# Performance work log

Hardware: AMD Instinct MI355X
Metric: run time of the kernel (lower is better)

The kernel has to match this reference:

```python
import jax, jax.numpy as jnp
import numpy as np

B, S, N_ITEMS, E, H, L, DFF = 32, 512, 2048, 512, 8, 2, 2048
DK = E // H
EPS = 1e-5


def setup_inputs() -> dict:
    key = jax.random.key(0)
    ks = jax.random.split(key, 32)
    sc = 0.02
    p = {
        'input_seq': jax.random.normal(ks[0], (B, S, N_ITEMS), jnp.float32),
        'emb_W': jax.random.normal(ks[1], (N_ITEMS, E), jnp.float32) * sc,
        'emb_b': jnp.zeros((E,), jnp.float32),
        'pos_emb': jax.random.normal(ks[2], (S, E), jnp.float32) * sc,
        'Wq': jax.random.normal(ks[3], (L, E, E), jnp.float32) * sc,
        'bq': jnp.zeros((L, E), jnp.float32),
        'Wk': jax.random.normal(ks[4], (L, E, E), jnp.float32) * sc,
        'bk': jnp.zeros((L, E), jnp.float32),
        'Wv': jax.random.normal(ks[5], (L, E, E), jnp.float32) * sc,
        'bv': jnp.zeros((L, E), jnp.float32),
        'Wo': jax.random.normal(ks[6], (L, E, E), jnp.float32) * sc,
        'bo': jnp.zeros((L, E), jnp.float32),
        'ln1_g': jnp.ones((L, E), jnp.float32),
        'ln1_b': jnp.zeros((L, E), jnp.float32),
        'W1': jax.random.normal(ks[7], (L, E, DFF), jnp.float32) * sc,
        'b1': jnp.zeros((L, DFF), jnp.float32),
        'W2': jax.random.normal(ks[8], (L, DFF, E), jnp.float32) * sc,
        'b2': jnp.zeros((L, E), jnp.float32),
        'ln2_g': jnp.ones((L, E), jnp.float32),
        'ln2_b': jnp.zeros((L, E), jnp.float32),
        'fc_W': jax.random.normal(ks[9], (E, 1), jnp.float32) * sc,
        'fc_b': jnp.zeros((1,), jnp.float32),
    }
    return p


def _layernorm(x, g, b):
    m = jnp.mean(x, axis=-1, keepdims=True)
    v = jnp.mean(jnp.square(x - m), axis=-1, keepdims=True)
    return (x - m) * jax.lax.rsqrt(v + EPS) * g + b


def reference(input_seq, emb_W, emb_b, pos_emb, Wq, bq, Wk, bk, Wv, bv, Wo, bo,
              ln1_g, ln1_b, W1, b1, W2, b2, ln2_g, ln2_b, fc_W, fc_b):
    x = input_seq @ emb_W + emb_b          # [B,S,E]
    x = x + pos_emb[None, :, :]
    tril = jnp.tril(jnp.ones((S, S), jnp.float32))  # causal lower-triangular
    for l in range(L):
        # --- self attention (faithful: tril BEFORE scale, zeros not -inf) ---
        q = (x @ Wq[l] + bq[l]).reshape(B, S, H, DK).transpose(0, 2, 1, 3)
        k = (x @ Wk[l] + bk[l]).reshape(B, S, H, DK).transpose(0, 2, 1, 3)
        v = (x @ Wv[l] + bv[l]).reshape(B, S, H, DK).transpose(0, 2, 1, 3)
        scores = jnp.einsum('bhqd,bhkd->bhqk', q, k)
        scores = (scores * tril) / np.sqrt(DK)
        probs = jax.nn.softmax(scores, axis=-1)
        attn = jnp.einsum('bhqk,bhkd->bhqd', probs, v)  # [B,H,S,DK]
        attn = attn.transpose(0, 2, 1, 3).reshape(B, S, E)
        attn = attn @ Wo[l] + bo[l]
        # faithful source bug: `self_attention(x,x,x)[0]` -> batch 0 only,
        # broadcast over all batches in the residual add
        attended0 = attn[0]                 # [S,E]
        x = _layernorm(x + attended0[None, :, :], ln1_g[l], ln1_b[l])
        # --- feed forward ---
        ff = jax.nn.relu(x @ W1[l] + b1[l]) @ W2[l] + b2[l]
        x = _layernorm(x + ff, ln2_g[l], ln2_b[l])
    out = (x @ fc_W + fc_b).squeeze(-1)     # [B,S]
    return out
```

## Files before the change

### kernel.cpp

```cpp
#include <hip/hip_runtime.h>


typedef __bf16 bf16;
typedef __bf16 bf16x8 __attribute__((ext_vector_type(8)));
typedef __bf16 bf16x4 __attribute__((ext_vector_type(4)));
typedef float  f32x4  __attribute__((ext_vector_type(4)));

#define SEQ 512

__device__ __forceinline__ void gl2lds16(const bf16* g, void* l) {
    __builtin_amdgcn_global_load_lds(
        (const __attribute__((address_space(1))) void*)g,
        (__attribute__((address_space(3))) void*)l, 16, 0, 0);
}

template<int N> __device__ __forceinline__ void waitvm() {
    if constexpr (N == 0)      asm volatile("s_waitcnt vmcnt(0)" ::: "memory");
    else if constexpr (N == 2) asm volatile("s_waitcnt vmcnt(2)" ::: "memory");
    else if constexpr (N == 3) asm volatile("s_waitcnt vmcnt(3)" ::: "memory");
    else if constexpr (N == 4) asm volatile("s_waitcnt vmcnt(4)" ::: "memory");
    else if constexpr (N == 5) asm volatile("s_waitcnt vmcnt(5)" ::: "memory");
    else if constexpr (N == 6) asm volatile("s_waitcnt vmcnt(6)" ::: "memory");
    else if constexpr (N == 8) asm volatile("s_waitcnt vmcnt(8)" ::: "memory");
    else static_assert(N == 0, "unsupported waitvm");
}

__global__ __launch_bounds__(512, 1)
void fattn(const bf16* __restrict__ qkv,
           const bf16* __restrict__ VT,
           bf16* __restrict__ attn0b)
{
    __shared__ __align__(1024) char smem[65536 + 65536 + 8192];
    char* Ks = smem;
    char* Vs = smem + 65536;
    const int h = blockIdx.y;
    const int q0 = blockIdx.x * 128;
    const int tid = threadIdx.x, lane = tid & 63, wv = tid >> 6;
    const int fr = lane & 15, fc = lane >> 4;
    char* Ps = smem + 131072 + wv * 1024;

    {
        const bf16* Kg = qkv + 512 + h * 64;
        #pragma unroll
        for (int p = 0; p < 8; ++p) {
            int row = p * 64 + (tid >> 3);
            int ch  = tid & 7;
            gl2lds16(Kg + (long long)row * 1536 + ((ch ^ (row & 7)) * 8),
                     Ks + p * 8192 + tid * 16);
        }
        const bf16* Vg = VT + (long long)h * 64 * 512;
        #pragma unroll
        for (int p = 0; p < 8; ++p) {
            int row = p * 8 + (tid >> 6);
            int ch  = tid & 63;
            int chg = (ch & ~7) | ((ch & 7) ^ (row & 7));
            gl2lds16(Vg + (long long)row * 512 + chg * 8,
                     Vs + p * 8192 + tid * 16);
        }
    }
    const int q0w = q0 + wv * 16;
    const int qg  = q0w + fr;
    bf16x8 qf[2];
    #pragma unroll
    for (int w = 0; w < 2; ++w)
        qf[w] = *(const bf16x8*)(qkv + (long long)qg * 1536 + h * 64 + w * 32 + fc * 8);

    asm volatile("s_waitcnt vmcnt(0)" ::: "memory");
    __builtin_amdgcn_s_barrier();
    asm volatile("" ::: "memory");

    f32x4 s[32] = {};
    #pragma unroll
    for (int kt = 0; kt < 32; ++kt) {
        #pragma unroll
        for (int w = 0; w < 2; ++w) {
            int row = kt * 16 + fr;
            bf16x8 kf = *(const bf16x8*)(Ks + row * 128 +
                                         (((w * 4 + fc) ^ (row & 7)) * 16));
            s[kt] = __builtin_amdgcn_mfma_f32_16x16x32_bf16(kf, qf[w], s[kt], 0, 0, 0);
        }
    }

    float mx = -3.4e38f;
    #pragma unroll
    for (int kt = 0; kt < 32; ++kt)
        #pragma unroll
        for (int rr = 0; rr < 4; ++rr) {
            int k = kt * 16 + fc * 4 + rr;
            float v = (k <= qg) ? s[kt][rr] * 0.125f : 0.0f;
            s[kt][rr] = v;
            mx = fmaxf(mx, v);
        }
    mx = fmaxf(mx, __shfl_xor(mx, 16));
    mx = fmaxf(mx, __shfl_xor(mx, 32));
    float sum = 0.f;
    #pragma unroll
    for (int kt = 0; kt < 32; ++kt)
        #pragma unroll
        for (int rr = 0; rr < 4; ++rr) {
            float e = __expf(s[kt][rr] - mx);
            s[kt][rr] = e;
            sum += e;
        }
    sum += __shfl_xor(sum, 16);
    sum += __shfl_xor(sum, 32);
    const float inv = 1.0f / sum;

    f32x4 o[4] = {};
    #pragma unroll
    for (int kt2 = 0; kt2 < 16; ++kt2) {
        bf16x4 u0, u1;
        #pragma unroll
        for (int rr = 0; rr < 4; ++rr) {
            u0[rr] = (bf16)(s[2 * kt2][rr] * inv);
            u1[rr] = (bf16)(s[2 * kt2 + 1][rr] * inv);
        }
        *(bf16x4*)(Ps + fr * 64 + ((fc ^ (fr & 7)) * 8))       = u0;
        *(bf16x4*)(Ps + fr * 64 + (((4 + fc) ^ (fr & 7)) * 8)) = u1;
        __threadfence_block();
        bf16x4 lo = *(const bf16x4*)(Ps + fr * 64 + (((2 * fc) ^ (fr & 7)) * 8));
        bf16x4 hi = *(const bf16x4*)(Ps + fr * 64 + (((2 * fc + 1) ^ (fr & 7)) * 8));
        bf16x8 pf;
        pf[0] = lo[0]; pf[1] = lo[1]; pf[2] = lo[2]; pf[3] = lo[3];
        pf[4] = hi[0]; pf[5] = hi[1]; pf[6] = hi[2]; pf[7] = hi[3];
        #pragma unroll
        for (int n = 0; n < 4; ++n) {
            int row = n * 16 + fr;
            int ch  = kt2 * 4 + fc;
            int chs = (ch & ~7) | ((ch & 7) ^ (row & 7));
            bf16x8 vf = *(const bf16x8*)(Vs + row * 1024 + chs * 16);
            o[n] = __builtin_amdgcn_mfma_f32_16x16x32_bf16(pf, vf, o[n], 0, 0, 0);
        }
    }

    #pragma unroll
    for (int n = 0; n < 4; ++n)
        #pragma unroll
        for (int rr = 0; rr < 4; ++rr) {
            int qrow = q0w + fc * 4 + rr;
            attn0b[(long long)qrow * 512 + h * 64 + n * 16 + fr] = (bf16)o[n][rr];
        }
}

template<int BN, int ACT, int POS>
__global__ __launch_bounds__(512, 1)
void mg8(const bf16* __restrict__ Ab, int lda,
         const bf16* __restrict__ Bt, int ldb,
         const float* __restrict__ bias, const float* __restrict__ pos,
         bf16* __restrict__ Cb, int ldc, int K)
{
    constexpr int BM = 256;
    constexpr int APASS = 2;
    constexpr int BPASS = BN / 128;
    constexpr int AHB = BM * 64;
    constexpr int BHB = BN * 64;
    constexpr int WM = (BN == 256 ? 2 : 4), WN = 8 / WM;
    constexpr int MR = BM / WM / 16;
    constexpr int NR = BN / WN / 16;
    __shared__ __align__(1024) char smem[4 * AHB + 4 * BHB];
    char* ABase = smem;
    char* BBase = smem + 4 * AHB;

    const int gx = gridDim.x, gy = gridDim.y;
    const int nwg = gx * gy;
    const int b = blockIdx.y * gx + blockIdx.x;
    const int q = nwg >> 3, r = nwg & 7;
    const int xcd = b & 7, loc = b >> 3;
    const int wg = (xcd < r ? xcd * (q + 1) : r * (q + 1) + (xcd - r) * q) + loc;
    const int bx = wg % gx, by = wg / gx;
    const int row0 = by * BM, col0 = bx * BN;

    const int tid = threadIdx.x, lane = tid & 63, wv = tid >> 6;
    const int wr = (WM == 2 ? (wv >> 2) : (wv >> 1));
    const int wc = (WM == 2 ? (wv & 3) : (wv & 1));
    const int fr = lane & 15, fc = lane >> 4;

    const bf16* aS[APASS];
    #pragma unroll
    for (int p = 0; p < APASS; ++p) {
        int cL = p * 512 + tid;
        int row = cL >> 2, ch = cL & 3;
        aS[p] = Ab + (long long)(row0 + row) * lda + ((ch ^ (row & 3)) * 8);
    }
    const bf16* bS[BPASS];
    #pragma unroll
    for (int p = 0; p < BPASS; ++p) {
        int cL = p * 512 + tid;
        int row = cL >> 2, ch = cL & 3;
        bS[p] = Bt + (long long)(col0 + row) * ldb + ((ch ^ (row & 3)) * 8);
    }
    int aOff[MR], bOff[NR];
    #pragma unroll
    for (int m = 0; m < MR; ++m) {
        int row = wr * (BM / WM) + m * 16 + fr;
        aOff[m] = row * 64 + ((fc ^ (row & 3)) * 16);
    }
    #pragma unroll
    for (int n = 0; n < NR; ++n) {
        int row = wc * (BN / WN) + n * 16 + fr;
        bOff[n] = row * 64 + ((fc ^ (row & 3)) * 16);
    }

    auto stagePart = [&](int j) {
        const int tau = j >> 2, kh = (j >> 1) & 1, d = tau & 1;
        const int koff = tau * 64 + kh * 32;
        if (!(j & 1)) {
            char* dst = ABase + (d * 2 + kh) * AHB + wv * 1024;
            #pragma unroll
            for (int p = 0; p < APASS; ++p)
                gl2lds16(aS[p] + koff, dst + p * 8192);
        } else {
            char* dst = BBase + (d * 2 + kh) * BHB + wv * 1024;
            #pragma unroll
            for (int p = 0; p < BPASS; ++p)
                gl2lds16(bS[p] + koff, dst + p * 8192);
        }
    };

    const int nt = K >> 6;
    const int T = 4 * nt;
    #pragma unroll
    for (int j = 0; j < 6; ++j)
        if (j < T) stagePart(j);
    waitvm<2 * (APASS + BPASS)>();
    __builtin_amdgcn_s_barrier();

    f32x4 acc[MR][NR] = {};
    const int NPH = 2 * nt;
    for (int g = 0; g < NPH; ++g) {
        const int tau = g >> 1, ks = g & 1, d = tau & 1;

        const char* as = ABase + (d * 2 + ks) * AHB;
        const char* bs = BBase + (d * 2 + ks) * BHB;
        bf16x8 a[MR], b2[NR];
        #pragma unroll
        for (int m = 0; m < MR; ++m) a[m] = *(const bf16x8*)(as + aOff[m]);
        #pragma unroll
        for (int n = 0; n < NR; ++n) b2[n] = *(const bf16x8*)(bs + bOff[n]);

        if (2 * g + 6 < T) stagePart(2 * g + 6);
        if (2 * g + 7 < T) stagePart(2 * g + 7);

        __builtin_amdgcn_s_setprio(1);
        #pragma unroll
        for (int m = 0; m < MR; ++m)
            #pragma unroll
            for (int n = 0; n < NR; ++n)
                acc[m][n] = __builtin_amdgcn_mfma_f32_16x16x32_bf16(
                    a[m], b2[n], acc[m][n], 0, 0, 0);
        __builtin_amdgcn_s_setprio(0);

        const int rem = T - (2 * g + 4);
        if (rem >= 4)      waitvm<2 * (APASS + BPASS)>();
        else if (rem == 3) waitvm<2 * APASS + BPASS>();
        else if (rem == 2) waitvm<APASS + BPASS>();
        else if (rem == 1) waitvm<APASS>();
        else               waitvm<0>();
        __builtin_amdgcn_s_barrier();
    }

    float* st = (float*)(smem + wv * 4096);
    const int rowb = row0 + wr * (BM / WM);
    const int colb = col0 + wc * (BN / WN);
    #pragma unroll
    for (int m = 0; m < MR; ++m) {
        #pragma unroll
        for (int n = 0; n < NR; ++n) {
            int col = colb + n * 16 + fr;
            float bb = bias ? bias[col] : 0.f;
            #pragma unroll
            for (int rr = 0; rr < 4; ++rr) {
                float x = acc[m][n][rr] + bb;
                if constexpr (POS) {
                    int rowg = rowb + m * 16 + fc * 4 + rr;
                    x += pos[(rowg & 511) * 512 + col];
                }
                if constexpr (ACT) x = fmaxf(x, 0.f);
                st[(fc * 4 + rr) * 64 + n * 16 + fr] = x;
            }
        }
        #pragma unroll
        for (int sgi = 0; sgi < 2; ++sgi) {
            int row = sgi * 8 + (lane >> 3);
            int c8 = (lane & 7) * 8;
            f32x4 u = *(const f32x4*)&st[row * 64 + c8];
            f32x4 v = *(const f32x4*)&st[row * 64 + c8 + 4];
            bf16x8 w8;
            w8[0] = (bf16)u[0]; w8[1] = (bf16)u[1];
            w8[2] = (bf16)u[2]; w8[3] = (bf16)u[3];
            w8[4] = (bf16)v[0]; w8[5] = (bf16)v[1];
            w8[6] = (bf16)v[2]; w8[7] = (bf16)v[3];
            *(bf16x8*)&Cb[(long long)(rowb + m * 16 + row) * ldc + colb + c8] = w8;
        }
    }
}

template<int BM, int BN, int ACT, int CMODE, int CAUSAL>
__global__ __launch_bounds__(256, 4)
void mgemm(const bf16* __restrict__ Ab, int lda, long long sA,
           const bf16* __restrict__ Bt, int ldb, long long sB,
           const float* __restrict__ bias,
           float* __restrict__ Cf, bf16* __restrict__ Cb, int ldc, long long sC,
           int K)
{
    static_assert(BM == 128 && (BN == 128 || BN == 64), "tile");
    const int gx = gridDim.x, gy = gridDim.y;
    const int nwg = gx * gy;
    const int b = blockIdx.y * gx + blockIdx.x;
    const int q = nwg >> 3, r = nwg & 7;
    const int xcd = b & 7, loc = b >> 3;
    const int wg = (xcd < r ? xcd * (q + 1) : r * (q + 1) + (xcd - r) * q) + loc;
    const int bx = wg % gx, by = wg / gx;
    if (CAUSAL && bx * BN > by * BM + (BM - 1)) return;

    constexpr int TM = BM / 32, TN = BN / 32;
    constexpr int AIT = BM / 64, BIT = BN / 64;
    constexpr int ABY = BM * 64;
    constexpr int BBY = BN * 64;
    __shared__ bf16 As[2 * BM * 32];
    __shared__ bf16 Bs[2 * BN * 32];
    char* AsB = (char*)As;
    char* BsB = (char*)Bs;
    const int tid = threadIdx.x;
    const int lane = tid & 63, wv = tid >> 6;
    const int wr = wv >> 1, wc = wv & 1;
    const int fr = lane & 15, fc = lane >> 4;
    const int row0 = by * BM, col0 = bx * BN;
    const int z = blockIdx.z;

    Ab += (long long)z * sA;
    Bt += (long long)z * sB;
    if constexpr (CMODE == 0) Cf += (long long)z * sC;
    else                      Cb += (long long)z * sC;

    f32x4 acc[TM][TN] = {};

    const bf16* aSrc[AIT];
    #pragma unroll
    for (int it = 0; it < AIT; ++it) {
        int cL = it * 256 + tid;
        int row = cL >> 2, ch = cL & 3;
        aSrc[it] = Ab + (long long)(row0 + row) * lda + ((ch ^ (row & 3)) * 8);
    }
    const bf16* bSrc[BIT];
    #pragma unroll
    for (int it = 0; it < BIT; ++it) {
        int cL = it * 256 + tid;
        int row = cL >> 2, ch = cL & 3;
        bSrc[it] = Bt + (long long)(col0 + row) * ldb + ((ch ^ (row & 3)) * 8);
    }
    int aOff[TM], bOff[TN];
    #pragma unroll
    for (int m = 0; m < TM; ++m) {
        int row = wr * (BM / 2) + m * 16 + fr;
        aOff[m] = row * 64 + ((fc ^ (row & 3)) * 16);
    }
    #pragma unroll
    for (int n = 0; n < TN; ++n) {
        int row = wc * (BN / 2) + n * 16 + fr;
        bOff[n] = row * 64 + ((fc ^ (row & 3)) * 16);
    }

    auto stageTo = [&](int buf, int kt) {
        #pragma unroll
        for (int it = 0; it < AIT; ++it)
            gl2lds16(aSrc[it] + kt, AsB + buf * ABY + it * 4096 + wv * 1024);
        #pragma unroll
        for (int it = 0; it < BIT; ++it)
            gl2lds16(bSrc[it] + kt, BsB + buf * BBY + it * 4096 + wv * 1024);
    };

    const int nt = K >> 5;
    stageTo(0, 0);
    asm volatile("s_waitcnt vmcnt(0)" ::: "memory");
    __builtin_amdgcn_s_barrier();
    asm volatile("" ::: "memory");

    int cur = 0;
    for (int t = 0; t < nt; ++t) {
        if (t + 1 < nt) stageTo(cur ^ 1, (t + 1) * 32);
        bf16x8 a[TM], b2[TN];
        #pragma unroll
        for (int m = 0; m < TM; ++m) a[m] = *(const bf16x8*)(AsB + cur * ABY + aOff[m]);
        #pragma unroll
        for (int n = 0; n < TN; ++n) b2[n] = *(const bf16x8*)(BsB + cur * BBY + bOff[n]);
        __builtin_amdgcn_s_setprio(1);
        #pragma unroll
        for (int m = 0; m < TM; ++m)
            #pragma unroll
            for (int n = 0; n < TN; ++n)
                acc[m][n] = __builtin_amdgcn_mfma_f32_16x16x32_bf16(a[m], b2[n], acc[m][n], 0, 0, 0);
        __builtin_amdgcn_s_setprio(0);
        if (t + 1 < nt) {
            asm volatile("s_waitcnt vmcnt(0)" ::: "memory");
            __builtin_amdgcn_s_barrier();
            asm volatile("" ::: "memory");
            cur ^= 1;
        }
    }

    #pragma unroll
    for (int n = 0; n < TN; ++n) {
        int col = col0 + wc * (BN / 2) + n * 16 + fr;
        float bb = bias ? bias[col] : 0.f;
        #pragma unroll
        for (int m = 0; m < TM; ++m) {
            int rbase = row0 + wr * (BM / 2) + m * 16 + fc * 4;
            #pragma unroll
            for (int rr = 0; rr < 4; ++rr) {
                float x = acc[m][n][rr] + bb;
                if constexpr (ACT) x = fmaxf(x, 0.f);
                long long ci = (long long)(rbase + rr) * ldc + col;
                if constexpr (CMODE == 0) Cf[ci] = x;
                else                      Cb[ci] = (bf16)x;
            }
        }
    }
}

__global__ __launch_bounds__(256)
void cvt_k(const float* __restrict__ in, bf16* __restrict__ outb, long long n8)
{
    long long i = (long long)blockIdx.x * 256 + threadIdx.x;
    const long long stride = (long long)gridDim.x * 256;
    for (; i < n8; i += stride) {
        const float* p = in + i * 8;
        float4 u = *(const float4*)p;
        float4 v = *(const float4*)(p + 4);
        bf16x8 w8;
        w8[0] = (bf16)u.x; w8[1] = (bf16)u.y; w8[2] = (bf16)u.z; w8[3] = (bf16)u.w;
        w8[4] = (bf16)v.x; w8[5] = (bf16)v.y; w8[6] = (bf16)v.z; w8[7] = (bf16)v.w;
        *(bf16x8*)(outb + i * 8) = w8;
    }
}

__global__ __launch_bounds__(256)
void wt_k(const float* __restrict__ W, bf16* __restrict__ WT, int K, int N)
{
    __shared__ float t[32][33];
    int n0 = blockIdx.x * 32, k0 = blockIdx.y * 32;
    int r = threadIdx.x >> 3, c4 = (threadIdx.x & 7) * 4;
    float4 v = *(const float4*)&W[(long long)(k0 + r) * N + n0 + c4];
    t[r][c4 + 0] = v.x; t[r][c4 + 1] = v.y;
    t[r][c4 + 2] = v.z; t[r][c4 + 3] = v.w;
    __syncthreads();
    int n = threadIdx.x >> 3, kk4 = (threadIdx.x & 7) * 4;
    bf16x4 o;
    o[0] = (bf16)t[kk4 + 0][n]; o[1] = (bf16)t[kk4 + 1][n];
    o[2] = (bf16)t[kk4 + 2][n]; o[3] = (bf16)t[kk4 + 3][n];
    *(bf16x4*)&WT[(long long)(n0 + n) * K + k0 + kk4] = o;
}

__global__ __launch_bounds__(512)
void packb_k(const float* __restrict__ bq, const float* __restrict__ bk,
             const float* __restrict__ bv, float* __restrict__ dst)
{
    int l = blockIdx.x, t = threadIdx.x;
    dst[l * 1536 + t]        = bq[l * 512 + t];
    dst[l * 1536 + 512 + t]  = bk[l * 512 + t];
    dst[l * 1536 + 1024 + t] = bv[l * 512 + t];
}

__global__ __launch_bounds__(256)
void vt_k(const bf16* __restrict__ qkv, bf16* __restrict__ VT)
{
    __shared__ bf16 t[64][80];
    int h = blockIdx.y, s0 = blockIdx.x * 64;
    int r = threadIdx.x >> 2, c16 = (threadIdx.x & 3) * 16;
    const bf16* src = qkv + (long long)(s0 + r) * 1536 + 1024 + h * 64 + c16;
    *(bf16x8*)&t[r][c16]     = *(const bf16x8*)src;
    *(bf16x8*)&t[r][c16 + 8] = *(const bf16x8*)(src + 8);
    __syncthreads();
    int d = r, seg = c16;
    bf16 tmp[16];
    #pragma unroll
    for (int j = 0; j < 16; ++j) tmp[j] = t[seg + j][d];
    bf16* dst = VT + ((long long)(h * 64 + d)) * 512 + s0 + seg;
    *(bf16x8*)dst       = *(bf16x8*)&tmp[0];
    *(bf16x8*)(dst + 8) = *(bf16x8*)&tmp[8];
}

__global__ __launch_bounds__(128)
void addln_k(bf16* __restrict__ xb, const bf16* __restrict__ res,
             unsigned resMask, const float* __restrict__ g,
             const float* __restrict__ bta)
{
    long long row = blockIdx.x;
    int tid = threadIdx.x;
    int c = tid * 4;
    bf16x4 xv4 = *(const bf16x4*)&xb[row * 512 + c];
    bf16x4 rv4 = *(const bf16x4*)&res[(long long)(blockIdx.x & resMask) * 512 + c];
    float x0 = (float)xv4[0] + (float)rv4[0];
    float x1 = (float)xv4[1] + (float)rv4[1];
    float x2 = (float)xv4[2] + (float)rv4[2];
    float x3 = (float)xv4[3] + (float)rv4[3];
    float s = x0 + x1 + x2 + x3;
    float qq = x0 * x0 + x1 * x1 + x2 * x2 + x3 * x3;
    #pragma unroll
    for (int off = 32; off; off >>= 1) {
        s += __shfl_xor(s, off);
        qq += __shfl_xor(qq, off);
    }
    __shared__ float rs[2], rq[2];
    if ((tid & 63) == 0) { rs[tid >> 6] = s; rq[tid >> 6] = qq; }
    __syncthreads();
    s = rs[0] + rs[1]; qq = rq[0] + rq[1];
    float mean = s * (1.0f / 512.0f);
    float var  = qq * (1.0f / 512.0f) - mean * mean;
    float rstd = rsqrtf(var + 1e-5f);
    float4 gv = *(const float4*)&g[c];
    float4 bv = *(const float4*)&bta[c];
    bf16x4 o4;
    o4[0] = (bf16)((x0 - mean) * rstd * gv.x + bv.x);
    o4[1] = (bf16)((x1 - mean) * rstd * gv.y + bv.y);
    o4[2] = (bf16)((x2 - mean) * rstd * gv.z + bv.z);
    o4[3] = (bf16)((x3 - mean) * rstd * gv.w + bv.w);
    *(bf16x4*)&xb[row * 512 + c] = o4;
}

__global__ __launch_bounds__(256)
void fc_k(const bf16* __restrict__ x, const float* __restrict__ w,
          const float* __restrict__ bb, float* __restrict__ out)
{
    int row  = blockIdx.x * 4 + (threadIdx.x >> 6);
    int lane = threadIdx.x & 63;
    const bf16* xr = x + (long long)row * 512;
    bf16x8 a8 = *(const bf16x8*)&xr[lane * 8];
    float4 w0 = *(const float4*)&w[lane * 8];
    float4 w1 = *(const float4*)&w[lane * 8 + 4];
    float s = (float)a8[0] * w0.x + (float)a8[1] * w0.y
            + (float)a8[2] * w0.z + (float)a8[3] * w0.w
            + (float)a8[4] * w1.x + (float)a8[5] * w1.y
            + (float)a8[6] * w1.z + (float)a8[7] * w1.w;
    #pragma unroll
    for (int off = 32; off; off >>= 1) s += __shfl_xor(s, off);
    if (lane == 0) out[row] = s + bb[0];
}

extern "C" void kernel_launch(void* const* d_in, const int* in_sizes, int n_in,
                              void* d_out, int out_size, void* d_ws, size_t ws_size,
                              hipStream_t stream)
{
    const float* input_seq = (const float*)d_in[0];
    const float* emb_W  = (const float*)d_in[1];
    const float* emb_b  = (const float*)d_in[2];
    const float* pos_emb= (const float*)d_in[3];
    const float* Wq = (const float*)d_in[4];
    const float* bq = (const float*)d_in[5];
    const float* Wk = (const float*)d_in[6];
    const float* bk = (const float*)d_in[7];
    const float* Wv = (const float*)d_in[8];
    const float* bv = (const float*)d_in[9];
    const float* Wo = (const float*)d_in[10];
    const float* bo = (const float*)d_in[11];
    const float* ln1_g = (const float*)d_in[12];
    const float* ln1_b = (const float*)d_in[13];
    const float* W1 = (const float*)d_in[14];
    const float* b1 = (const float*)d_in[15];
    const float* W2 = (const float*)d_in[16];
    const float* b2 = (const float*)d_in[17];
    const float* ln2_g = (const float*)d_in[18];
    const float* ln2_b = (const float*)d_in[19];
    const float* fcW = (const float*)d_in[20];
    const float* fcb = (const float*)d_in[21];
    float* out = (float*)d_out;

    char* w = (char*)d_ws;
    size_t off = 0;
    auto alloc = [&](size_t bytes) -> void* {
        off = (off + 255) & ~(size_t)255;
        void* p = w + off;
        off += bytes;
        return p;
    };
    bf16*  xb     = (bf16*) alloc(16384ull * 512 * 2);
    bf16*  embWT  = (bf16*) alloc(512ull * 2048 * 2);
    bf16*  qkvWT  = (bf16*) alloc(2ull * 1536 * 512 * 2);
    bf16*  WoT    = (bf16*) alloc(2ull * 512 * 512 * 2);
    bf16*  W1T    = (bf16*) alloc(2ull * 2048 * 512 * 2);
    bf16*  W2T    = (bf16*) alloc(2ull * 512 * 2048 * 2);
    float* qkvB   = (float*)alloc(2ull * 1536 * 4);
    off = (off + 255) & ~(size_t)255;
    char* dynp = w + off;
    bf16*  seqb     = (bf16*)dynp;
    bf16*  qkv      = (bf16*)dynp;
    bf16*  VT       = (bf16*)(dynp + 1572864);
    bf16*  attn0b   = (bf16*)(dynp + 1572864 + 524288);
    bf16*  attnout0b= (bf16*)(dynp + 1572864 + 524288 + 524288);
    bf16*  hidden = (bf16*)dynp;
    bf16*  ffout  = (bf16*)(dynp + 16384ull * 2048 * 2);

    dim3 blk(256);
    dim3 blk512(512);

    wt_k<<<dim3(16, 64), blk, 0, stream>>>(emb_W, embWT, 2048, 512);
    for (int l = 0; l < 2; ++l) {
        wt_k<<<dim3(16, 16), blk, 0, stream>>>(Wq + l * 262144, qkvWT + l * 786432,          512, 512);
        wt_k<<<dim3(16, 16), blk, 0, stream>>>(Wk + l * 262144, qkvWT + l * 786432 + 262144, 512, 512);
        wt_k<<<dim3(16, 16), blk, 0, stream>>>(Wv + l * 262144, qkvWT + l * 786432 + 524288, 512, 512);
        wt_k<<<dim3(16, 16), blk, 0, stream>>>(Wo + l * 262144, WoT + l * 262144, 512, 512);
        wt_k<<<dim3(64, 16), blk, 0, stream>>>(W1 + l * 1048576, W1T + l * 1048576, 512, 2048);
        wt_k<<<dim3(16, 64), blk, 0, stream>>>(W2 + l * 1048576, W2T + l * 1048576, 2048, 512);
    }
    packb_k<<<dim3(2), dim3(512), 0, stream>>>(bq, bk, bv, qkvB);
    cvt_k<<<dim3(2048), blk, 0, stream>>>(input_seq, seqb, 16384ll * 2048 / 8);

    mg8<128, 0, 1><<<dim3(4, 64), blk512, 0, stream>>>(
        seqb, 2048, embWT, 2048, emb_b, pos_emb, xb, 512, 2048);

    for (int l = 0; l < 2; ++l) {
        const bf16* qkvWT_l = qkvWT + l * 786432;
        const bf16* WoT_l   = WoT + l * 262144;
        const bf16* W1T_l   = W1T + l * 1048576;
        const bf16* W2T_l   = W2T + l * 1048576;

        mgemm<128, 128, 0, 1, 0><<<dim3(12, 4), blk, 0, stream>>>(
            xb, 512, 0, qkvWT_l, 512, 0, qkvB + l * 1536,
            nullptr, qkv, 1536, 0, 512);
        vt_k<<<dim3(8, 8), blk, 0, stream>>>(qkv, VT);
        fattn<<<dim3(4, 8), blk512, 0, stream>>>(qkv, VT, attn0b);
        mgemm<128, 128, 0, 1, 0><<<dim3(4, 4), blk, 0, stream>>>(
            attn0b, 512, 0, WoT_l, 512, 0, bo + l * 512, nullptr,
            attnout0b, 512, 0, 512);
        addln_k<<<dim3(16384), dim3(128), 0, stream>>>(
            xb, attnout0b, 511u, ln1_g + l * 512, ln1_b + l * 512);

        mg8<256, 1, 0><<<dim3(8, 64), blk512, 0, stream>>>(
            xb, 512, W1T_l, 512, b1 + l * 2048, nullptr, hidden, 2048, 512);
        mg8<128, 0, 0><<<dim3(4, 64), blk512, 0, stream>>>(
            hidden, 2048, W2T_l, 2048, b2 + l * 512, nullptr, ffout, 512, 2048);
        addln_k<<<dim3(16384), dim3(128), 0, stream>>>(
            xb, ffout, 0xffffffffu, ln2_g + l * 512, ln2_b + l * 512);
    }

    fc_k<<<dim3(4096), blk, 0, stream>>>(xb, fcW, fcb, out);
}
```

Before: 402.2 us.

## Fuse weight-prep launches into one kernel and shrink attention GEMM tiles

Merges the thirteen weight-transpose launches, the bias pack and the input fp32-to-bf16 conversion into a single table-driven kernel, so per-launch overhead and the tail gaps between many small kernels go away. It also halves the N tile of the QKV and output-projection GEMMs on the batch-0 path, which doubles their block counts so more CUs are busy on these small problems. The cost is a per-block lookup over the table and smaller tiles with less data reuse per block.

```diff
diff --git a/kernel.cpp b/kernel.cpp
--- a/kernel.cpp
+++ b/kernel.cpp
@@ -23,6 +23,67 @@
     else if constexpr (N == 6) asm volatile("s_waitcnt vmcnt(6)" ::: "memory");
     else if constexpr (N == 8) asm volatile("s_waitcnt vmcnt(8)" ::: "memory");
     else static_assert(N == 0, "unsupported waitvm");
+}
+
+struct WTab {
+    const float* src[13];
+    bf16*        dst[13];
+    int          K[13];
+    int          N[13];
+    int          base[13];
+    const float *bq, *bk, *bv;
+    float*       qkvB;
+    const float* cvtsrc;
+    bf16*        cvtdst;
+};
+
+__global__ __launch_bounds__(256)
+void wtall_k(WTab tab, int nTiles)
+{
+    const int b = blockIdx.x;
+    if (b < nTiles) {
+        int mi = 0;
+        #pragma unroll
+        for (int i = 1; i < 13; ++i)
+            if (b >= tab.base[i]) mi = i;
+        const int lt = b - tab.base[mi];
+        const int K = tab.K[mi], N = tab.N[mi];
+        const int tx = N >> 5;
+        const int n0 = (lt % tx) * 32, k0 = (lt / tx) * 32;
+        const float* W = tab.src[mi];
+        bf16* WT = tab.dst[mi];
+        __shared__ float t[32][33];
+        int r = threadIdx.x >> 3, c4 = (threadIdx.x & 7) * 4;
+        float4 v = *(const float4*)&W[(long long)(k0 + r) * N + n0 + c4];
+        t[r][c4 + 0] = v.x; t[r][c4 + 1] = v.y;
+        t[r][c4 + 2] = v.z; t[r][c4 + 3] = v.w;
+        __syncthreads();
+        int n = threadIdx.x >> 3, kk4 = (threadIdx.x & 7) * 4;
+        bf16x4 o;
+        o[0] = (bf16)t[kk4 + 0][n]; o[1] = (bf16)t[kk4 + 1][n];
+        o[2] = (bf16)t[kk4 + 2][n]; o[3] = (bf16)t[kk4 + 3][n];
+        *(bf16x4*)&WT[(long long)(n0 + n) * K + k0 + kk4] = o;
+    } else if (b < nTiles + 2) {
+        const int l = b - nTiles;
+        for (int t2 = threadIdx.x; t2 < 512; t2 += 256) {
+            tab.qkvB[l * 1536 + t2]        = tab.bq[l * 512 + t2];
+            tab.qkvB[l * 1536 + 512 + t2]  = tab.bk[l * 512 + t2];
+            tab.qkvB[l * 1536 + 1024 + t2] = tab.bv[l * 512 + t2];
+        }
+    } else {
+        long long i = (long long)(b - nTiles - 2) * 256 + threadIdx.x;
+        const long long stride = 2048ll * 256;
+        const long long n8 = 16384ll * 2048 / 8;
+        for (; i < n8; i += stride) {
+            const float* p = tab.cvtsrc + i * 8;
+            float4 u = *(const float4*)p;
+            float4 v = *(const float4*)(p + 4);
+            bf16x8 w8;
+            w8[0] = (bf16)u.x; w8[1] = (bf16)u.y; w8[2] = (bf16)u.z; w8[3] = (bf16)u.w;
+            w8[4] = (bf16)v.x; w8[5] = (bf16)v.y; w8[6] = (bf16)v.z; w8[7] = (bf16)v.w;
+            *(bf16x8*)(tab.cvtdst + i * 8) = w8;
+        }
+    }
 }
 
 __global__ __launch_bounds__(512, 1)
@@ -416,49 +477,6 @@
             }
         }
     }
-}
-
-__global__ __launch_bounds__(256)
-void cvt_k(const float* __restrict__ in, bf16* __restrict__ outb, long long n8)
-{
-    long long i = (long long)blockIdx.x * 256 + threadIdx.x;
-    const long long stride = (long long)gridDim.x * 256;
-    for (; i < n8; i += stride) {
-        const float* p = in + i * 8;
-        float4 u = *(const float4*)p;
-        float4 v = *(const float4*)(p + 4);
-        bf16x8 w8;
-        w8[0] = (bf16)u.x; w8[1] = (bf16)u.y; w8[2] = (bf16)u.z; w8[3] = (bf16)u.w;
-        w8[4] = (bf16)v.x; w8[5] = (bf16)v.y; w8[6] = (bf16)v.z; w8[7] = (bf16)v.w;
-        *(bf16x8*)(outb + i * 8) = w8;
-    }
-}
-
-__global__ __launch_bounds__(256)
-void wt_k(const float* __restrict__ W, bf16* __restrict__ WT, int K, int N)
-{
-    __shared__ float t[32][33];
-    int n0 = blockIdx.x * 32, k0 = blockIdx.y * 32;
-    int r = threadIdx.x >> 3, c4 = (threadIdx.x & 7) * 4;
-    float4 v = *(const float4*)&W[(long long)(k0 + r) * N + n0 + c4];
-    t[r][c4 + 0] = v.x; t[r][c4 + 1] = v.y;
-    t[r][c4 + 2] = v.z; t[r][c4 + 3] = v.w;
-    __syncthreads();
-    int n = threadIdx.x >> 3, kk4 = (threadIdx.x & 7) * 4;
-    bf16x4 o;
-    o[0] = (bf16)t[kk4 + 0][n]; o[1] = (bf16)t[kk4 + 1][n];
-    o[2] = (bf16)t[kk4 + 2][n]; o[3] = (bf16)t[kk4 + 3][n];
-    *(bf16x4*)&WT[(long long)(n0 + n) * K + k0 + kk4] = o;
-}
-
-__global__ __launch_bounds__(512)
-void packb_k(const float* __restrict__ bq, const float* __restrict__ bk,
-             const float* __restrict__ bv, float* __restrict__ dst)
-{
-    int l = blockIdx.x, t = threadIdx.x;
-    dst[l * 1536 + t]        = bq[l * 512 + t];
-    dst[l * 1536 + 512 + t]  = bk[l * 512 + t];
-    dst[l * 1536 + 1024 + t] = bv[l * 512 + t];
 }
 
 __global__ __launch_bounds__(256)
@@ -593,17 +611,29 @@
     dim3 blk(256);
     dim3 blk512(512);
 
-    wt_k<<<dim3(16, 64), blk, 0, stream>>>(emb_W, embWT, 2048, 512);
-    for (int l = 0; l < 2; ++l) {
-        wt_k<<<dim3(16, 16), blk, 0, stream>>>(Wq + l * 262144, qkvWT + l * 786432,          512, 512);
-        wt_k<<<dim3(16, 16), blk, 0, stream>>>(Wk + l * 262144, qkvWT + l * 786432 + 262144, 512, 512);
-        wt_k<<<dim3(16, 16), blk, 0, stream>>>(Wv + l * 262144, qkvWT + l * 786432 + 524288, 512, 512);
-        wt_k<<<dim3(16, 16), blk, 0, stream>>>(Wo + l * 262144, WoT + l * 262144, 512, 512);
-        wt_k<<<dim3(64, 16), blk, 0, stream>>>(W1 + l * 1048576, W1T + l * 1048576, 512, 2048);
-        wt_k<<<dim3(16, 64), blk, 0, stream>>>(W2 + l * 1048576, W2T + l * 1048576, 2048, 512);
-    }
-    packb_k<<<dim3(2), dim3(512), 0, stream>>>(bq, bk, bv, qkvB);
-    cvt_k<<<dim3(2048), blk, 0, stream>>>(input_seq, seqb, 16384ll * 2048 / 8);
+    WTab tab;
+    int nTiles = 0;
+    {
+        int idx = 0;
+        auto add = [&](const float* s, bf16* d, int K, int N) {
+            tab.src[idx] = s; tab.dst[idx] = d;
+            tab.K[idx] = K; tab.N[idx] = N; tab.base[idx] = nTiles;
+            nTiles += (K / 32) * (N / 32);
+            ++idx;
+        };
+        add(emb_W, embWT, 2048, 512);
+        for (int l = 0; l < 2; ++l) {
+            add(Wq + l * 262144, qkvWT + l * 786432,          512, 512);
+            add(Wk + l * 262144, qkvWT + l * 786432 + 262144, 512, 512);
+            add(Wv + l * 262144, qkvWT + l * 786432 + 524288, 512, 512);
+            add(Wo + l * 262144, WoT + l * 262144,            512, 512);
+            add(W1 + l * 1048576, W1T + l * 1048576,          512, 2048);
+            add(W2 + l * 1048576, W2T + l * 1048576,          2048, 512);
+        }
+        tab.bq = bq; tab.bk = bk; tab.bv = bv; tab.qkvB = qkvB;
+        tab.cvtsrc = input_seq; tab.cvtdst = seqb;
+    }
+    wtall_k<<<dim3(nTiles + 2 + 2048), blk, 0, stream>>>(tab, nTiles);
 
     mg8<128, 0, 1><<<dim3(4, 64), blk512, 0, stream>>>(
         seqb, 2048, embWT, 2048, emb_b, pos_emb, xb, 512, 2048);
@@ -614,12 +644,12 @@
         const bf16* W1T_l   = W1T + l * 1048576;
         const bf16* W2T_l   = W2T + l * 1048576;
 
-        mgemm<128, 128, 0, 1, 0><<<dim3(12, 4), blk, 0, stream>>>(
+        mgemm<128, 64, 0, 1, 0><<<dim3(24, 4), blk, 0, stream>>>(
             xb, 512, 0, qkvWT_l, 512, 0, qkvB + l * 1536,
             nullptr, qkv, 1536, 0, 512);
         vt_k<<<dim3(8, 8), blk, 0, stream>>>(qkv, VT);
         fattn<<<dim3(4, 8), blk512, 0, stream>>>(qkv, VT, attn0b);
-        mgemm<128, 128, 0, 1, 0><<<dim3(4, 4), blk, 0, stream>>>(
+        mgemm<128, 64, 0, 1, 0><<<dim3(8, 4), blk, 0, stream>>>(
             attn0b, 512, 0, WoT_l, 512, 0, bo + l * 512, nullptr,
             attnout0b, 512, 0, 512);
         addln_k<<<dim3(16384), dim3(128), 0, stream>>>(
```

Measured after the change: 363.3 us. -9.7%, faster.
